# Kernel optimization log

Hardware: AMD Instinct MI355X
Metric: run time of the kernel (lower is better)

Reference implementation:

```python
import jax, jax.numpy as jnp
import numpy as np

H, W = 4096, 4096
KH, KW = 15, 15


def setup_inputs() -> dict:
    key = jax.random.key(0)
    k1, k2 = jax.random.split(key)
    x = jax.random.normal(k1, (H, W), dtype=jnp.float32)
    weight = jax.random.normal(k2, (KH, KW), dtype=jnp.float32)
    bias = jnp.zeros((1,), dtype=jnp.float32)
    return {"x": x, "weight": weight, "bias": bias}


def reference(x, weight, bias):
    # corr2d: valid cross-correlation of 2D x with 2D kernel, output [H-KH+1, W-KW+1]
    # lax conv with NCHW/OIHW layout computes cross-correlation (no kernel flip),
    # identical to the torch per-pixel slice-multiply-sum loop.
    out = jax.lax.conv_general_dilated(
        x[None, None, :, :],            # [1,1,H,W]
        weight[None, None, :, :],       # [1,1,KH,KW]
        window_strides=(1, 1),
        padding="VALID",
    )[0, 0]                             # [H-KH+1, W-KW+1]
    return out + bias  # bias is shape [1], broadcasts like torch
```

## Files before the change

kernel.cpp:

```cpp
#include <hip/hip_runtime.h>


#define HIN 4096
#define WIN 4096
#define KH 15
#define KW 15
#define OH (HIN - KH + 1)
#define OW (WIN - KW + 1)

#define BX 64
#define BY 64
#define XROWS (BY + KH - 1)
#define XCOLS 80
#define LDSW 88
#define NSH (XROWS * LDSW)
#define NB4 (XCOLS / 4)
#define NITEM (XROWS * NB4)

typedef short bf16x8 __attribute__((ext_vector_type(8)));
typedef float f32x4  __attribute__((ext_vector_type(4)));

static __device__ inline short f2bf(float f) {
    unsigned u = __float_as_uint(f);
    u += 0x7fffu + ((u >> 16) & 1u);
    return (short)(u >> 16);
}

__global__ void conv2d_btab(const float* __restrict__ w, short* __restrict__ btab) {
    const int e = blockIdx.x * 256 + threadIdx.x;
    if (e >= KH * 64) return;
    const int kh = e >> 6;
    const int L  = e & 63;
    const int n  = L & 15;
    const int q  = L >> 4;
    bf16x8 bv;
#pragma unroll
    for (int j = 0; j < 8; ++j) {
        const int d = q * 8 + j - n;
        bv[j] = (d >= 0 && d < KW) ? f2bf(w[kh * KW + d]) : (short)0;
    }
    *reinterpret_cast<bf16x8*>(&btab[(size_t)e * 8]) = bv;
}

__global__ __launch_bounds__(256, 8)
void conv2d_mfma(const float* __restrict__ x,
                 const short* __restrict__ btab,
                 const float* __restrict__ bias,
                 float* __restrict__ out) {
    __shared__ short lds[NSH];

    const int tid = threadIdx.x;
    const int ox0 = blockIdx.x * BX;
    const int oy0 = blockIdx.y * BY;

    if (ox0 + XCOLS <= WIN && oy0 + XROWS <= HIN) {
        float4 v[7];
#pragma unroll
        for (int i = 0; i < 7; ++i) {
            const int f = tid + 256 * i;
            if (f < NITEM) {
                const int r  = f / NB4;
                const int c4 = (f - r * NB4) * 4;
                v[i] = *reinterpret_cast<const float4*>(&x[(size_t)(oy0 + r) * WIN + ox0 + c4]);
            }
        }
#pragma unroll
        for (int i = 0; i < 7; ++i) {
            const int f = tid + 256 * i;
            if (f < NITEM) {
                const int r  = f / NB4;
                const int c4 = (f - r * NB4) * 4;
                short4 s;
                s.x = f2bf(v[i].x); s.y = f2bf(v[i].y);
                s.z = f2bf(v[i].z); s.w = f2bf(v[i].w);
                *reinterpret_cast<short4*>(&lds[r * LDSW + c4]) = s;
            }
        }
    } else {
        for (int f = tid; f < NITEM; f += 256) {
            const int r  = f / NB4;
            const int c4 = (f - r * NB4) * 4;
            int gy = oy0 + r;
            if (gy > HIN - 1) gy = HIN - 1;
            const int gx = ox0 + c4;
            float4 v;
            if (gx + 3 <= WIN - 1) {
                v = *reinterpret_cast<const float4*>(&x[(size_t)gy * WIN + gx]);
            } else {
                const float* row = &x[(size_t)gy * WIN];
                const int x0 = (gx + 0 > WIN - 1) ? WIN - 1 : gx + 0;
                const int x1 = (gx + 1 > WIN - 1) ? WIN - 1 : gx + 1;
                const int x2 = (gx + 2 > WIN - 1) ? WIN - 1 : gx + 2;
                const int x3 = (gx + 3 > WIN - 1) ? WIN - 1 : gx + 3;
                v = make_float4(row[x0], row[x1], row[x2], row[x3]);
            }
            short4 s;
            s.x = f2bf(v.x); s.y = f2bf(v.y); s.z = f2bf(v.z); s.w = f2bf(v.w);
            *reinterpret_cast<short4*>(&lds[r * LDSW + c4]) = s;
        }
    }
    __syncthreads();

    const int lane = tid & 63;
    const int wv   = tid >> 6;
    const int m    = lane & 15;
    const int q    = lane >> 4;

    f32x4 acc[4];
#pragma unroll
    for (int t = 0; t < 4; ++t) acc[t] = (f32x4){0.f, 0.f, 0.f, 0.f};

    const short*  abase = &lds[(wv * 16 + m) * LDSW + q * 8];
    const bf16x8* bt    = reinterpret_cast<const bf16x8*>(btab) + lane;
#pragma unroll
    for (int kh = 0; kh < KH; ++kh) {
        const bf16x8 b = bt[kh * 64];
#pragma unroll
        for (int t = 0; t < 4; ++t) {
            const bf16x8 a =
                *reinterpret_cast<const bf16x8*>(abase + kh * LDSW + t * 16);
            acc[t] = __builtin_amdgcn_mfma_f32_16x16x32_bf16(a, b, acc[t], 0, 0, 0);
        }
    }

    const float b0 = bias[0];
    const int row0 = oy0 + wv * 16 + q * 4;
#pragma unroll
    for (int t = 0; t < 4; ++t) {
        const int col = ox0 + t * 16 + m;
        if (col < OW) {
#pragma unroll
            for (int r = 0; r < 4; ++r) {
                const int row = row0 + r;
                if (row < OH)
                    out[(size_t)row * OW + col] = acc[t][r] + b0;
            }
        }
    }
}

extern "C" void kernel_launch(void* const* d_in, const int* in_sizes, int n_in,
                              void* d_out, int out_size, void* d_ws, size_t ws_size,
                              hipStream_t stream) {
    const float* x    = (const float*)d_in[0];
    const float* w    = (const float*)d_in[1];
    const float* bias = (const float*)d_in[2];
    float* out        = (float*)d_out;
    short* btab       = (short*)d_ws;

    conv2d_btab<<<dim3((KH * 64 + 255) / 256), dim3(256), 0, stream>>>(w, btab);

    dim3 grid((OW + BX - 1) / BX, (OH + BY - 1) / BY);
    dim3 block(256);
    conv2d_mfma<<<grid, block, 0, stream>>>(x, btab, bias, out);
}
```

Measured before the change: 138.2 us.

## Switch conv to 32x32x16 MFMA tiles with taller 128-row blocks

Replaces the per-wave four 16x16x32 MFMAs per kernel row with three 32x32x16 MFMAs over a 32x32 output tile, and rebuilds the banded weight table to match the new operand layout. The block grows to 512 threads covering 128 output rows, so the halo rows loaded per output row shrink. The intent is to cut MFMA issue count and redundant halo loads and conversions. In exchange it uses more LDS per block and larger blocks, which can lower occupancy, and the 32-column band is zero-padded across three K slices.

```diff
diff --git a/kernel.cpp b/kernel.cpp
--- a/kernel.cpp
+++ b/kernel.cpp
@@ -9,16 +9,17 @@
 #define OW (WIN - KW + 1)
 
 #define BX 64
-#define BY 64
+#define BY 128
 #define XROWS (BY + KH - 1)
 #define XCOLS 80
 #define LDSW 88
 #define NSH (XROWS * LDSW)
 #define NB4 (XCOLS / 4)
 #define NITEM (XROWS * NB4)
+#define NTHR 512
 
-typedef short bf16x8 __attribute__((ext_vector_type(8)));
-typedef float f32x4  __attribute__((ext_vector_type(4)));
+typedef short bf16x8  __attribute__((ext_vector_type(8)));
+typedef float f32x16  __attribute__((ext_vector_type(16)));
 
 static __device__ inline short f2bf(float f) {
     unsigned u = __float_as_uint(f);
@@ -28,21 +29,22 @@
 
 __global__ void conv2d_btab(const float* __restrict__ w, short* __restrict__ btab) {
     const int e = blockIdx.x * 256 + threadIdx.x;
-    if (e >= KH * 64) return;
-    const int kh = e >> 6;
+    if (e >= KH * 3 * 64) return;
+    const int kh = e / (3 * 64);
+    const int s  = (e >> 6) % 3;
     const int L  = e & 63;
-    const int n  = L & 15;
-    const int q  = L >> 4;
+    const int n  = L & 31;
+    const int h  = L >> 5;
     bf16x8 bv;
 #pragma unroll
     for (int j = 0; j < 8; ++j) {
-        const int d = q * 8 + j - n;
+        const int d = 16 * s + h * 8 + j - n;
         bv[j] = (d >= 0 && d < KW) ? f2bf(w[kh * KW + d]) : (short)0;
     }
     *reinterpret_cast<bf16x8*>(&btab[(size_t)e * 8]) = bv;
 }
 
-__global__ __launch_bounds__(256, 8)
+__global__ __launch_bounds__(NTHR, 8)
 void conv2d_mfma(const float* __restrict__ x,
                  const short* __restrict__ btab,
                  const float* __restrict__ bias,
@@ -54,10 +56,10 @@
     const int oy0 = blockIdx.y * BY;
 
     if (ox0 + XCOLS <= WIN && oy0 + XROWS <= HIN) {
-        float4 v[7];
+        float4 v[6];
 #pragma unroll
-        for (int i = 0; i < 7; ++i) {
-            const int f = tid + 256 * i;
+        for (int i = 0; i < 6; ++i) {
+            const int f = tid + NTHR * i;
             if (f < NITEM) {
                 const int r  = f / NB4;
                 const int c4 = (f - r * NB4) * 4;
@@ -65,8 +67,8 @@
             }
         }
 #pragma unroll
-        for (int i = 0; i < 7; ++i) {
-            const int f = tid + 256 * i;
+        for (int i = 0; i < 6; ++i) {
+            const int f = tid + NTHR * i;
             if (f < NITEM) {
                 const int r  = f / NB4;
                 const int c4 = (f - r * NB4) * 4;
@@ -77,7 +79,7 @@
             }
         }
     } else {
-        for (int f = tid; f < NITEM; f += 256) {
+        for (int f = tid; f < NITEM; f += NTHR) {
             const int r  = f / NB4;
             const int c4 = (f - r * NB4) * 4;
             int gy = oy0 + r;
@@ -101,40 +103,37 @@
     }
     __syncthreads();
 
-    const int lane = tid & 63;
-    const int wv   = tid >> 6;
-    const int m    = lane & 15;
-    const int q    = lane >> 4;
+    const int lane  = tid & 63;
+    const int wv    = tid >> 6;
+    const int ctile = (wv & 1) * 32;
+    const int rtile = (wv >> 1) * 32;
+    const int m     = lane & 31;
+    const int h     = lane >> 5;
 
-    f32x4 acc[4];
-#pragma unroll
-    for (int t = 0; t < 4; ++t) acc[t] = (f32x4){0.f, 0.f, 0.f, 0.f};
+    f32x16 acc = (f32x16){0.f};
 
-    const short*  abase = &lds[(wv * 16 + m) * LDSW + q * 8];
+    const short*  abase = &lds[(rtile + m) * LDSW + ctile + h * 8];
     const bf16x8* bt    = reinterpret_cast<const bf16x8*>(btab) + lane;
 #pragma unroll
     for (int kh = 0; kh < KH; ++kh) {
-        const bf16x8 b = bt[kh * 64];
 #pragma unroll
-        for (int t = 0; t < 4; ++t) {
+        for (int s = 0; s < 3; ++s) {
+            const bf16x8 b = bt[(kh * 3 + s) * 64];
             const bf16x8 a =
-                *reinterpret_cast<const bf16x8*>(abase + kh * LDSW + t * 16);
-            acc[t] = __builtin_amdgcn_mfma_f32_16x16x32_bf16(a, b, acc[t], 0, 0, 0);
+                *reinterpret_cast<const bf16x8*>(abase + kh * LDSW + s * 16);
+            acc = __builtin_amdgcn_mfma_f32_32x32x16_bf16(a, b, acc, 0, 0, 0);
         }
     }
 
-    const float b0 = bias[0];
-    const int row0 = oy0 + wv * 16 + q * 4;
+    const float b0  = bias[0];
+    const int   col = ox0 + ctile + m;
+    const int   rw0 = oy0 + rtile + 4 * h;
+    if (col < OW) {
 #pragma unroll
-    for (int t = 0; t < 4; ++t) {
-        const int col = ox0 + t * 16 + m;
-        if (col < OW) {
-#pragma unroll
-            for (int r = 0; r < 4; ++r) {
-                const int row = row0 + r;
-                if (row < OH)
-                    out[(size_t)row * OW + col] = acc[t][r] + b0;
-            }
+        for (int reg = 0; reg < 16; ++reg) {
+            const int row = rw0 + (reg & 3) + 8 * (reg >> 2);
+            if (row < OH)
+                out[(size_t)row * OW + col] = acc[reg] + b0;
         }
     }
 }
@@ -148,9 +147,9 @@
     float* out        = (float*)d_out;
     short* btab       = (short*)d_ws;
 
-    conv2d_btab<<<dim3((KH * 64 + 255) / 256), dim3(256), 0, stream>>>(w, btab);
+    conv2d_btab<<<dim3((KH * 3 * 64 + 255) / 256), dim3(256), 0, stream>>>(w, btab);
 
     dim3 grid((OW + BX - 1) / BX, (OH + BY - 1) / BY);
-    dim3 block(256);
+    dim3 block(NTHR);
     conv2d_mfma<<<grid, block, 0, stream>>>(x, btab, bias, out);
 }
```

After: 151.0 us. +9.3%, slower.

## Give each wavefront a private LDS halo tile and drop block barrier

Applied to the files above, without the earlier changes.

Each of the four wavefronts now loads its own 30-row halo window into a private LDS slice and computes its 16 output rows without a block-wide __syncthreads. This removes the cross-wave barrier so waves can run MFMA as soon as their own data lands. In exchange, each block loads 120 input rows instead of 78, roughly doubling LDS use and global/L2 read traffic, and the occupancy hint drops from 8 to 6 blocks per SIMD group.

```diff
diff --git a/kernel.cpp b/kernel.cpp
--- a/kernel.cpp
+++ b/kernel.cpp
@@ -10,12 +10,13 @@
 
 #define BX 64
 #define BY 64
-#define XROWS (BY + KH - 1)
+#define WROWS 30
 #define XCOLS 80
 #define LDSW 88
-#define NSH (XROWS * LDSW)
-#define NB4 (XCOLS / 4)
-#define NITEM (XROWS * NB4)
+#define WSH (WROWS * LDSW)
+#define NSH (4 * WSH)
+#define WNB4 (XCOLS / 4)
+#define WNITEM (WROWS * WNB4)
 
 typedef short bf16x8 __attribute__((ext_vector_type(8)));
 typedef float f32x4  __attribute__((ext_vector_type(4)));
@@ -42,45 +43,53 @@
     *reinterpret_cast<bf16x8*>(&btab[(size_t)e * 8]) = bv;
 }
 
-__global__ __launch_bounds__(256, 8)
+__global__ __launch_bounds__(256, 6)
 void conv2d_mfma(const float* __restrict__ x,
                  const short* __restrict__ btab,
                  const float* __restrict__ bias,
                  float* __restrict__ out) {
     __shared__ short lds[NSH];
 
-    const int tid = threadIdx.x;
-    const int ox0 = blockIdx.x * BX;
-    const int oy0 = blockIdx.y * BY;
+    const int tid  = threadIdx.x;
+    const int lane = tid & 63;
+    const int wv   = tid >> 6;
+    const int ox0  = blockIdx.x * BX;
+    const int oy0  = blockIdx.y * BY;
+    const int gy0  = oy0 + wv * 16;
 
-    if (ox0 + XCOLS <= WIN && oy0 + XROWS <= HIN) {
-        float4 v[7];
+    short* wlds = &lds[wv * WSH];
+
+    if (ox0 + XCOLS <= WIN && gy0 + WROWS <= HIN) {
 #pragma unroll
-        for (int i = 0; i < 7; ++i) {
-            const int f = tid + 256 * i;
-            if (f < NITEM) {
-                const int r  = f / NB4;
-                const int c4 = (f - r * NB4) * 4;
-                v[i] = *reinterpret_cast<const float4*>(&x[(size_t)(oy0 + r) * WIN + ox0 + c4]);
+        for (int half = 0; half < 2; ++half) {
+            float4 v[5];
+#pragma unroll
+            for (int i = 0; i < 5; ++i) {
+                const int f = lane + 64 * (half * 5 + i);
+                if (f < WNITEM) {
+                    const int r  = f / WNB4;
+                    const int c4 = (f - r * WNB4) * 4;
+                    v[i] = *reinterpret_cast<const float4*>(&x[(size_t)(gy0 + r) * WIN + ox0 + c4]);
+                }
             }
-        }
 #pragma unroll
-        for (int i = 0; i < 7; ++i) {
-            const int f = tid + 256 * i;
-            if (f < NITEM) {
-                const int r  = f / NB4;
-                const int c4 = (f - r * NB4) * 4;
-                short4 s;
-                s.x = f2bf(v[i].x); s.y = f2bf(v[i].y);
-                s.z = f2bf(v[i].z); s.w = f2bf(v[i].w);
-                *reinterpret_cast<short4*>(&lds[r * LDSW + c4]) = s;
+            for (int i = 0; i < 5; ++i) {
+                const int f = lane + 64 * (half * 5 + i);
+                if (f < WNITEM) {
+                    const int r  = f / WNB4;
+                    const int c4 = (f - r * WNB4) * 4;
+                    short4 s;
+                    s.x = f2bf(v[i].x); s.y = f2bf(v[i].y);
+                    s.z = f2bf(v[i].z); s.w = f2bf(v[i].w);
+                    *reinterpret_cast<short4*>(&wlds[r * LDSW + c4]) = s;
+                }
             }
         }
     } else {
-        for (int f = tid; f < NITEM; f += 256) {
-            const int r  = f / NB4;
-            const int c4 = (f - r * NB4) * 4;
-            int gy = oy0 + r;
+        for (int f = lane; f < WNITEM; f += 64) {
+            const int r  = f / WNB4;
+            const int c4 = (f - r * WNB4) * 4;
+            int gy = gy0 + r;
             if (gy > HIN - 1) gy = HIN - 1;
             const int gx = ox0 + c4;
             float4 v;
@@ -96,21 +105,18 @@
             }
             short4 s;
             s.x = f2bf(v.x); s.y = f2bf(v.y); s.z = f2bf(v.z); s.w = f2bf(v.w);
-            *reinterpret_cast<short4*>(&lds[r * LDSW + c4]) = s;
+            *reinterpret_cast<short4*>(&wlds[r * LDSW + c4]) = s;
         }
     }
-    __syncthreads();
 
-    const int lane = tid & 63;
-    const int wv   = tid >> 6;
-    const int m    = lane & 15;
-    const int q    = lane >> 4;
+    const int m = lane & 15;
+    const int q = lane >> 4;
 
     f32x4 acc[4];
 #pragma unroll
     for (int t = 0; t < 4; ++t) acc[t] = (f32x4){0.f, 0.f, 0.f, 0.f};
 
-    const short*  abase = &lds[(wv * 16 + m) * LDSW + q * 8];
+    const short*  abase = &wlds[m * LDSW + q * 8];
     const bf16x8* bt    = reinterpret_cast<const bf16x8*>(btab) + lane;
 #pragma unroll
     for (int kh = 0; kh < KH; ++kh) {
@@ -124,7 +130,7 @@
     }
 
     const float b0 = bias[0];
-    const int row0 = oy0 + wv * 16 + q * 4;
+    const int row0 = gy0 + q * 4;
 #pragma unroll
     for (int t = 0; t < 4; ++t) {
         const int col = ox0 + t * 16 + m;
```

New measurement: 144.2 us. 4.4% more time.

## Make conv blocks persistent over row tiles with double-buffered LDS prefetch

Applied to the files above, without the earlier changes.

Each block now handles four row tiles strided by a 16-row grid instead of one, which cuts the grid fourfold. The global loads for the next tile are issued into registers before the MFMA work on the current tile, then converted to bf16 and written into a second LDS buffer, so memory latency overlaps with compute. The cost is double the LDS, more registers (launch bounds lowered to 4 waves per SIMD), and fewer blocks for the GPU to schedule.

```diff
diff --git a/kernel.cpp b/kernel.cpp
--- a/kernel.cpp
+++ b/kernel.cpp
@@ -16,6 +16,8 @@
 #define NSH (XROWS * LDSW)
 #define NB4 (XCOLS / 4)
 #define NITEM (XROWS * NB4)
+#define TJ 4
+#define GRIDY 16
 
 typedef short bf16x8 __attribute__((ext_vector_type(8)));
 typedef float f32x4  __attribute__((ext_vector_type(4)));
@@ -42,99 +44,119 @@
     *reinterpret_cast<bf16x8*>(&btab[(size_t)e * 8]) = bv;
 }
 
-__global__ __launch_bounds__(256, 8)
+__global__ __launch_bounds__(256, 4)
 void conv2d_mfma(const float* __restrict__ x,
                  const short* __restrict__ btab,
                  const float* __restrict__ bias,
                  float* __restrict__ out) {
-    __shared__ short lds[NSH];
+    __shared__ short lds[2][NSH];
 
     const int tid = threadIdx.x;
     const int ox0 = blockIdx.x * BX;
-    const int oy0 = blockIdx.y * BY;
+    const bool xedge = (ox0 + XCOLS > WIN);
 
-    if (ox0 + XCOLS <= WIN && oy0 + XROWS <= HIN) {
-        float4 v[7];
+    int fr[7], fc[7];
+#pragma unroll
+    for (int i = 0; i < 7; ++i) {
+        const int f = tid + 256 * i;
+        fr[i] = f / NB4;
+        fc[i] = (f - fr[i] * NB4) * 4;
+    }
+    const bool v6 = (tid + 256 * 6) < NITEM;
+
+    float4 v[7];
+
+    auto stage_issue = [&](int iy0) {
+        if (!xedge) {
+#pragma unroll
+            for (int i = 0; i < 7; ++i) {
+                if (i < 6 || v6) {
+                    int gy = iy0 + fr[i];
+                    if (gy > HIN - 1) gy = HIN - 1;
+                    v[i] = *reinterpret_cast<const float4*>(&x[(size_t)gy * WIN + ox0 + fc[i]]);
+                }
+            }
+        } else {
+#pragma unroll
+            for (int i = 0; i < 7; ++i) {
+                if (i < 6 || v6) {
+                    int gy = iy0 + fr[i];
+                    if (gy > HIN - 1) gy = HIN - 1;
+                    const float* row = &x[(size_t)gy * WIN];
+                    const int gx = ox0 + fc[i];
+                    const int x0 = (gx + 0 > WIN - 1) ? WIN - 1 : gx + 0;
+                    const int x1 = (gx + 1 > WIN - 1) ? WIN - 1 : gx + 1;
+                    const int x2 = (gx + 2 > WIN - 1) ? WIN - 1 : gx + 2;
+                    const int x3 = (gx + 3 > WIN - 1) ? WIN - 1 : gx + 3;
+                    v[i] = make_float4(row[x0], row[x1], row[x2], row[x3]);
+                }
+            }
+        }
+    };
+    auto stage_write = [&](short* buf) {
 #pragma unroll
         for (int i = 0; i < 7; ++i) {
-            const int f = tid + 256 * i;
-            if (f < NITEM) {
-                const int r  = f / NB4;
-                const int c4 = (f - r * NB4) * 4;
-                v[i] = *reinterpret_cast<const float4*>(&x[(size_t)(oy0 + r) * WIN + ox0 + c4]);
-            }
-        }
-#pragma unroll
-        for (int i = 0; i < 7; ++i) {
-            const int f = tid + 256 * i;
-            if (f < NITEM) {
-                const int r  = f / NB4;
-                const int c4 = (f - r * NB4) * 4;
+            if (i < 6 || v6) {
                 short4 s;
                 s.x = f2bf(v[i].x); s.y = f2bf(v[i].y);
                 s.z = f2bf(v[i].z); s.w = f2bf(v[i].w);
-                *reinterpret_cast<short4*>(&lds[r * LDSW + c4]) = s;
+                *reinterpret_cast<short4*>(&buf[fr[i] * LDSW + fc[i]]) = s;
             }
         }
-    } else {
-        for (int f = tid; f < NITEM; f += 256) {
-            const int r  = f / NB4;
-            const int c4 = (f - r * NB4) * 4;
-            int gy = oy0 + r;
-            if (gy > HIN - 1) gy = HIN - 1;
-            const int gx = ox0 + c4;
-            float4 v;
-            if (gx + 3 <= WIN - 1) {
-                v = *reinterpret_cast<const float4*>(&x[(size_t)gy * WIN + gx]);
-            } else {
-                const float* row = &x[(size_t)gy * WIN];
-                const int x0 = (gx + 0 > WIN - 1) ? WIN - 1 : gx + 0;
-                const int x1 = (gx + 1 > WIN - 1) ? WIN - 1 : gx + 1;
-                const int x2 = (gx + 2 > WIN - 1) ? WIN - 1 : gx + 2;
-                const int x3 = (gx + 3 > WIN - 1) ? WIN - 1 : gx + 3;
-                v = make_float4(row[x0], row[x1], row[x2], row[x3]);
-            }
-            short4 s;
-            s.x = f2bf(v.x); s.y = f2bf(v.y); s.z = f2bf(v.z); s.w = f2bf(v.w);
-            *reinterpret_cast<short4*>(&lds[r * LDSW + c4]) = s;
-        }
-    }
-    __syncthreads();
+    };
 
     const int lane = tid & 63;
     const int wv   = tid >> 6;
     const int m    = lane & 15;
     const int q    = lane >> 4;
 
-    f32x4 acc[4];
+    const int     aoff = (wv * 16 + m) * LDSW + q * 8;
+    const bf16x8* bt   = reinterpret_cast<const bf16x8*>(btab) + lane;
+    const float   b0   = bias[0];
+
+    stage_issue(blockIdx.y * BY);
+    stage_write(&lds[0][0]);
+    __syncthreads();
+
 #pragma unroll
-    for (int t = 0; t < 4; ++t) acc[t] = (f32x4){0.f, 0.f, 0.f, 0.f};
+    for (int j = 0; j < TJ; ++j) {
+        const int oy0 = (blockIdx.y + GRIDY * j) * BY;
 
-    const short*  abase = &lds[(wv * 16 + m) * LDSW + q * 8];
-    const bf16x8* bt    = reinterpret_cast<const bf16x8*>(btab) + lane;
+        if (j + 1 < TJ)
+            stage_issue((blockIdx.y + GRIDY * (j + 1)) * BY);
+
+        const short* abase = &lds[j & 1][0] + aoff;
+        f32x4 acc[4];
 #pragma unroll
-    for (int kh = 0; kh < KH; ++kh) {
-        const bf16x8 b = bt[kh * 64];
+        for (int t = 0; t < 4; ++t) acc[t] = (f32x4){0.f, 0.f, 0.f, 0.f};
+#pragma unroll
+        for (int kh = 0; kh < KH; ++kh) {
+            const bf16x8 b = bt[kh * 64];
+#pragma unroll
+            for (int t = 0; t < 4; ++t) {
+                const bf16x8 a =
+                    *reinterpret_cast<const bf16x8*>(abase + kh * LDSW + t * 16);
+                acc[t] = __builtin_amdgcn_mfma_f32_16x16x32_bf16(a, b, acc[t], 0, 0, 0);
+            }
+        }
+
+        const int row0 = oy0 + wv * 16 + q * 4;
 #pragma unroll
         for (int t = 0; t < 4; ++t) {
-            const bf16x8 a =
-                *reinterpret_cast<const bf16x8*>(abase + kh * LDSW + t * 16);
-            acc[t] = __builtin_amdgcn_mfma_f32_16x16x32_bf16(a, b, acc[t], 0, 0, 0);
+            const int col = ox0 + t * 16 + m;
+            if (col < OW) {
+#pragma unroll
+                for (int r = 0; r < 4; ++r) {
+                    const int row = row0 + r;
+                    if (row < OH)
+                        out[(size_t)row * OW + col] = acc[t][r] + b0;
+                }
+            }
         }
-    }
 
-    const float b0 = bias[0];
-    const int row0 = oy0 + wv * 16 + q * 4;
-#pragma unroll
-    for (int t = 0; t < 4; ++t) {
-        const int col = ox0 + t * 16 + m;
-        if (col < OW) {
-#pragma unroll
-            for (int r = 0; r < 4; ++r) {
-                const int row = row0 + r;
-                if (row < OH)
-                    out[(size_t)row * OW + col] = acc[t][r] + b0;
-            }
+        if (j + 1 < TJ) {
+            stage_write(&lds[(j + 1) & 1][0]);
+            __syncthreads();
         }
     }
 }
@@ -150,7 +172,7 @@
 
     conv2d_btab<<<dim3((KH * 64 + 255) / 256), dim3(256), 0, stream>>>(w, btab);
 
-    dim3 grid((OW + BX - 1) / BX, (OH + BY - 1) / BY);
+    dim3 grid((OW + BX - 1) / BX, GRIDY);
     dim3 block(256);
     conv2d_mfma<<<grid, block, 0, stream>>>(x, btab, bias, out);
 }
```

After: 142.2 us. 1.03x slower.
